# Kernel optimization log

Hardware: AMD Instinct MI355X
Metric: run time of the kernel (lower is better)

The kernel has to match this reference:

```python
import jax, jax.numpy as jnp
import numpy as np

EPS = 1e-5

def layer_norm(x, w, b):
    mu = jnp.mean(x, axis=-1, keepdims=True)
    var = jnp.mean(jnp.square(x - mu), axis=-1, keepdims=True)
    return (x - mu) * jax.lax.rsqrt(var + EPS) * w + b

def setup_inputs() -> dict:
    key = jax.random.key(0)
    ks = jax.random.split(key, 8)
    B, T, C = 8, 512, 768
    s = 1.0 / np.sqrt(C)
    s4 = 1.0 / np.sqrt(4 * C)
    return {
        "x": jax.random.normal(ks[0], (B, T, C), dtype=jnp.float32),
        "ln1_w": jnp.ones((C,), jnp.float32),
        "ln1_b": jnp.zeros((C,), jnp.float32),
        "Wr": jax.random.normal(ks[1], (C, C), dtype=jnp.float32) * s,
        "Wk": jax.random.normal(ks[2], (C, C), dtype=jnp.float32) * s,
        "Wv": jax.random.normal(ks[3], (C, C), dtype=jnp.float32) * s,
        "time_mix_w": jnp.ones((C,), jnp.float32),  # torch init: torch.ones(n_embd)
        "Wrouter": jax.random.normal(ks[4], (C, C), dtype=jnp.float32) * s,
        "ln2_w": jnp.ones((C,), jnp.float32),
        "ln2_b": jnp.zeros((C,), jnp.float32),
        "Wck": jax.random.normal(ks[5], (4 * C, C), dtype=jnp.float32) * s,
        "Wcv": jax.random.normal(ks[6], (C, 4 * C), dtype=jnp.float32) * s4,
    }

def reference(x, ln1_w, ln1_b, Wr, Wk, Wv, time_mix_w, Wrouter, ln2_w, ln2_b, Wck, Wcv):
    B, T, C = x.shape
    xx = layer_norm(x, ln1_w, ln1_b)
    r = xx @ Wr.T
    k = xx @ Wk.T
    v = xx @ Wv.T
    w = -jnp.exp(time_mix_w)                        # (C,) negative per-channel decay rate
    idx = jnp.arange(T)
    diff = jnp.clip(idx[:, None] - idx[None, :], 0).astype(x.dtype)  # (T,T) t-j clamped at 0
    causal = jnp.tril(jnp.ones((T, T), x.dtype))
    decay = jnp.exp(w[:, None, None] * diff[None]) * causal          # (C,T,T)
    kv = k * v                                                       # (B,T,C)
    # wkv[b,t,c] = sum_j decay[c,t,j] * kv[b,j,c]
    wkv = jnp.einsum('ctj,bjc->btc', decay, kv)
    routed_wkv = wkv * jax.nn.sigmoid(xx @ Wrouter.T)
    x = x + r * routed_wkv
    xx2 = layer_norm(x, ln2_w, ln2_b)
    k_cm = jnp.square(jax.nn.relu(xx2 @ Wck.T))                      # (B,T,4C)
    return x + k_cm @ Wcv.T
```

## Files before the change

### kernel.cpp

```cpp
#include <hip/hip_runtime.h>
#include <hip/hip_bf16.h>

typedef __bf16 bf16_t;
typedef __bf16 bf16x8 __attribute__((ext_vector_type(8)));
typedef __bf16 bf16x4 __attribute__((ext_vector_type(4)));
typedef __bf16 bf16x2 __attribute__((ext_vector_type(2)));
typedef float  f32x4  __attribute__((ext_vector_type(4)));

#define LN_EPS 1e-5f


typedef __attribute__((address_space(1))) void gvoid_t;
typedef __attribute__((address_space(3))) void lvoid_t;
__device__ __forceinline__ void glds16(const void* g, void* l) {
    __builtin_amdgcn_global_load_lds((gvoid_t*)g, (lvoid_t*)l, 16, 0, 0);
}

__global__ __launch_bounds__(256) void k_cvt4(const float* __restrict__ s0,
                                              const float* __restrict__ s1,
                                              const float* __restrict__ s2,
                                              const float* __restrict__ s3,
                                              bf16_t* __restrict__ dst, int n4) {
    const float* s = (blockIdx.y == 0) ? s0 : (blockIdx.y == 1) ? s1 : (blockIdx.y == 2) ? s2 : s3;
    bf16_t* d = dst + (size_t)blockIdx.y * ((size_t)n4 * 4);
    int i = blockIdx.x * 256 + threadIdx.x;
    if (i < n4) {
        float4 v = ((const float4*)s)[i];
        bf16x4 o;
        o.x = (bf16_t)v.x; o.y = (bf16_t)v.y; o.z = (bf16_t)v.z; o.w = (bf16_t)v.w;
        ((bf16x4*)d)[i] = o;
    }
}

__global__ __launch_bounds__(256) void k_cvt2(const float* __restrict__ s0,
                                              const float* __restrict__ s1,
                                              bf16_t* __restrict__ dst, int n4) {
    const float* s = (blockIdx.y == 0) ? s0 : s1;
    bf16_t* d = dst + (size_t)blockIdx.y * ((size_t)n4 * 4);
    int i = blockIdx.x * 256 + threadIdx.x;
    if (i < n4) {
        float4 v = ((const float4*)s)[i];
        bf16x4 o;
        o.x = (bf16_t)v.x; o.y = (bf16_t)v.y; o.z = (bf16_t)v.z; o.w = (bf16_t)v.w;
        ((bf16x4*)d)[i] = o;
    }
}

__global__ __launch_bounds__(256) void k_ln(const float* __restrict__ x,
                                            const float* __restrict__ w,
                                            const float* __restrict__ b,
                                            bf16_t* __restrict__ out, int C) {
    int row = blockIdx.x;
    const float* xr = x + (long)row * C;
    int tid = threadIdx.x;
    float s = 0.f, s2 = 0.f;
    for (int i = tid; i < C; i += 256) { float v = xr[i]; s += v; s2 += v * v; }
    for (int m = 32; m; m >>= 1) { s += __shfl_xor(s, m, 64); s2 += __shfl_xor(s2, m, 64); }
    __shared__ float red[8];
    int wv = tid >> 6;
    if ((tid & 63) == 0) { red[wv] = s; red[4 + wv] = s2; }
    __syncthreads();
    float ts  = red[0] + red[1] + red[2] + red[3];
    float ts2 = red[4] + red[5] + red[6] + red[7];
    float mu  = ts / C;
    float var = ts2 / C - mu * mu;
    float rstd = rsqrtf(var + LN_EPS);
    bf16_t* orow = out + (long)row * C;
    for (int i = tid; i < C; i += 256)
        orow[i] = (bf16_t)((xr[i] - mu) * rstd * w[i] + b[i]);
}

template <int EPI>
__global__ __launch_bounds__(256, 6) void k_gemm_bt(const bf16_t* __restrict__ A,
                                                    const bf16_t* __restrict__ Bw,
                                                    void* __restrict__ Cout,
                                                    int N, int Ktot, int nbn, int nks) {
    constexpr int ABUF = 64 * 32;
    constexpr int BBUF = 128 * 32;
    __shared__ __align__(16) bf16_t As[2][64][32];
    __shared__ __align__(16) bf16_t Bs[2][128][32];
    const int tid  = threadIdx.x;
    const int lane = tid & 63, wid = tid >> 6;
    const int wm = (wid >> 1) * 32, wn = (wid & 1) * 64;

    int bid = blockIdx.x;
    int xcd = bid & 7, loc = bid >> 3;
    int bm  = (xcd >> 1) * 16 + loc / 12;
    int cix = (xcd & 1) * 12 + loc % 12;
    int ks  = cix / nbn;
    int bn  = cix % nbn;

    const int fr = lane & 15;
    const int swcol = (((lane >> 4) ^ (lane >> 2)) & 3) * 8;

    f32x4 acc[2][4];
#pragma unroll
    for (int i = 0; i < 2; i++)
#pragma unroll
        for (int j = 0; j < 4; j++) acc[i][j] = (f32x4){0.f, 0.f, 0.f, 0.f};

    const int rsub = lane >> 2;
    const int scol = (((lane & 3) ^ (lane >> 4)) & 3) * 8;
    const bf16_t* Ag = A  + (size_t)(bm * 64  + wid * 16 + rsub) * Ktot + (size_t)ks * 768 + scol;
    const bf16_t* Bg = Bw + (size_t)(bn * 128 + wid * 32 + rsub) * Ktot + (size_t)ks * 768 + scol;
    const size_t Kt16 = (size_t)16 * Ktot;
    bf16_t* lA = &As[0][wid * 16][0];
    bf16_t* lB = &Bs[0][wid * 32][0];

#define STAGE(buf, kt)                                            \
    do {                                                          \
        const bf16_t* a0 = Ag + (size_t)(kt) * 32;                \
        const bf16_t* b0 = Bg + (size_t)(kt) * 32;                \
        glds16(a0,        lA + (buf) * ABUF);                     \
        glds16(b0,        lB + (buf) * BBUF);                     \
        glds16(b0 + Kt16, lB + (buf) * BBUF + 16 * 32);           \
    } while (0)

#define COMPUTE(buf)                                                                         \
    do {                                                                                     \
        const bf16_t* pA = &As[0][0][0] + (buf) * ABUF + (wm + fr) * 32 + swcol;             \
        const bf16_t* pB = &Bs[0][0][0] + (buf) * BBUF + (wn + fr) * 32 + swcol;             \
        bf16x8 af[2], bfr[4];                                                                \
        _Pragma("unroll")                                                                    \
        for (int mi = 0; mi < 2; mi++) af[mi] = *(const bf16x8*)(pA + mi * 512);             \
        _Pragma("unroll")                                                                    \
        for (int ni = 0; ni < 4; ni++) bfr[ni] = *(const bf16x8*)(pB + ni * 512);            \
        __builtin_amdgcn_s_setprio(1);                                                       \
        _Pragma("unroll")                                                                    \
        for (int mi = 0; mi < 2; mi++)                                                       \
            _Pragma("unroll")                                                                \
            for (int ni = 0; ni < 4; ni++)                                                   \
                acc[mi][ni] = __builtin_amdgcn_mfma_f32_16x16x32_bf16(af[mi], bfr[ni], acc[mi][ni], 0, 0, 0); \
        __builtin_amdgcn_s_setprio(0);                                                       \
    } while (0)

    STAGE(0, 0);
    __syncthreads();
    int cur = 0;
    for (int kt = 0; kt < 23; ++kt) {
        STAGE(cur ^ 1, kt + 1);
        COMPUTE(cur);
        __syncthreads();
        cur ^= 1;
    }
    COMPUTE(cur);

#undef STAGE
#undef COMPUTE

    const int row0 = bm * 64 + wm, col0 = bn * 128 + wn;
#pragma unroll
    for (int mi = 0; mi < 2; mi++) {
#pragma unroll
        for (int ni = 0; ni < 4; ni++) {
            int row = row0 + mi * 16 + (lane >> 4) * 4;
            int col = col0 + ni * 16 + (lane & 15);
#pragma unroll
            for (int r = 0; r < 4; r++) {
                float val = acc[mi][ni][r];
                size_t off = (size_t)(row + r) * N + col;
                if (EPI == 0) {
                    ((bf16_t*)Cout)[off] = (bf16_t)val;
                } else if (EPI == 1) {
                    float t = fmaxf(val, 0.f);
                    ((bf16_t*)Cout)[off] = (bf16_t)(t * t);
                } else {
                    atomicAdd(&((float*)Cout)[off], val);
                }
            }
        }
    }
}

__global__ __launch_bounds__(256) void k_scan_local(const bf16_t* __restrict__ y4,
                                                    const float* __restrict__ tmw,
                                                    float* __restrict__ wkvl,
                                                    float* __restrict__ states) {
    int idx = blockIdx.x * 256 + threadIdx.x;
    int cp  = idx % 384;
    int rem = idx / 384;
    int ch  = rem & 15;
    int b   = rem >> 4;
    int c   = cp * 2;
    float d0 = expf(-expf(tmw[c]));
    float d1 = expf(-expf(tmw[c + 1]));
    const bf16_t* base = y4 + ((size_t)(b * 512 + ch * 32)) * 3072 + c;
    float*        wout = wkvl + ((size_t)(b * 512 + ch * 32)) * 768 + c;
    float s0 = 0.f, s1 = 0.f;
#pragma unroll 4
    for (int i = 0; i < 32; i++) {
        bf16x2 k2 = *(const bf16x2*)(base + (size_t)i * 3072 + 768);
        bf16x2 v2 = *(const bf16x2*)(base + (size_t)i * 3072 + 1536);
        s0 = s0 * d0 + (float)k2.x * (float)v2.x;
        s1 = s1 * d1 + (float)k2.y * (float)v2.y;
        *(float2*)(wout + (size_t)i * 768) = make_float2(s0, s1);
    }
    *(float2*)(states + ((size_t)(b * 16 + ch)) * 768 + c) = make_float2(s0, s1);
}

__global__ __launch_bounds__(256) void k_scan_carry(const float* __restrict__ states,
                                                    const float* __restrict__ tmw,
                                                    float* __restrict__ carries) {
    int idx = blockIdx.x * 256 + threadIdx.x;
    int c = idx % 768, b = idx / 768;
    float dL = expf(-expf(tmw[c]) * 32.f);
    float s = 0.f;
    for (int ch = 0; ch < 16; ch++) {
        size_t o = ((size_t)(b * 16 + ch)) * 768 + c;
        carries[o] = s;
        s = s * dL + states[o];
    }
}

__global__ __launch_bounds__(256) void k_mix_ln(const bf16_t* __restrict__ y4,
                                                const float* __restrict__ wkvl,
                                                const float* __restrict__ carries,
                                                const float* __restrict__ tmw,
                                                const float* __restrict__ x,
                                                const float* __restrict__ w2,
                                                const float* __restrict__ b2,
                                                float* __restrict__ out,
                                                bf16_t* __restrict__ xx2) {
    int bt = blockIdx.x;
    int t = bt & 511, b = bt >> 9;
    int tid = threadIdx.x;
    const bf16_t* yrow = y4 + (size_t)bt * 3072;
    const float*  wl   = wkvl + (size_t)bt * 768;
    const float*  cr   = carries + ((size_t)(b * 16) + (t >> 5)) * 768;
    const float*  xr   = x + (size_t)bt * 768;
    float tn = (float)((t & 31) + 1);

    float vals[3];
    float s = 0.f, s2 = 0.f;
#pragma unroll
    for (int j = 0; j < 3; j++) {
        int c = tid + j * 256;
        float rr = (float)yrow[c];
        float gg = (float)yrow[c + 2304];
        float wk = wl[c] + cr[c] * expf(-expf(tmw[c]) * tn);
        float sig = 1.f / (1.f + expf(-gg));
        float o = fmaf(rr, wk * sig, xr[c]);
        vals[j] = o; s += o; s2 += o * o;
    }
    for (int m = 32; m; m >>= 1) { s += __shfl_xor(s, m, 64); s2 += __shfl_xor(s2, m, 64); }
    __shared__ float red[8];
    int wv = tid >> 6;
    if ((tid & 63) == 0) { red[wv] = s; red[4 + wv] = s2; }
    __syncthreads();
    float ts  = red[0] + red[1] + red[2] + red[3];
    float ts2 = red[4] + red[5] + red[6] + red[7];
    float mu  = ts * (1.f / 768.f);
    float var = ts2 * (1.f / 768.f) - mu * mu;
    float rstd = rsqrtf(var + LN_EPS);
    float* orow = out + (size_t)bt * 768;
    bf16_t* xo = xx2 + (size_t)bt * 768;
#pragma unroll
    for (int j = 0; j < 3; j++) {
        int c = tid + j * 256;
        orow[c] = vals[j];
        xo[c] = (bf16_t)((vals[j] - mu) * rstd * w2[c] + b2[c]);
    }
}

extern "C" void kernel_launch(void* const* d_in, const int* in_sizes, int n_in,
                              void* d_out, int out_size, void* d_ws, size_t ws_size,
                              hipStream_t stream) {
    const float* x    = (const float*)d_in[0];
    const float* ln1w = (const float*)d_in[1];
    const float* ln1b = (const float*)d_in[2];
    const float* Wr   = (const float*)d_in[3];
    const float* Wk   = (const float*)d_in[4];
    const float* Wv   = (const float*)d_in[5];
    const float* tmw  = (const float*)d_in[6];
    const float* Wrt  = (const float*)d_in[7];
    const float* ln2w = (const float*)d_in[8];
    const float* ln2b = (const float*)d_in[9];
    const float* Wck  = (const float*)d_in[10];
    const float* Wcv  = (const float*)d_in[11];
    float* out = (float*)d_out;
    char* ws = (char*)d_ws;

    bf16_t* xx     = (bf16_t*)(ws + 0);
    bf16_t* wcat   = (bf16_t*)(ws + 6291456);
    bf16_t* wckb   = (bf16_t*)(ws + 11010048);
    bf16_t* wcvb   = (bf16_t*)(ws + 15728640);
    bf16_t* y4     = (bf16_t*)(ws + 20447232);
    bf16_t* kcm    = (bf16_t*)(ws + 20447232);
    float*  wkvl   = (float*)(ws + 70778880);
    float*  states = (float*)(ws + 83361792);
    float*  carr   = (float*)(ws + 83755008);

    const int n768 = 768 * 768 / 4;
    const int nbig = 3072 * 768 / 4;
    k_cvt4<<<dim3(576, 4), dim3(256), 0, stream>>>(Wr, Wk, Wv, Wrt, wcat, n768);
    k_cvt2<<<dim3(2304, 2), dim3(256), 0, stream>>>(Wck, Wcv, wckb, nbig);

    k_ln<<<dim3(4096), dim3(256), 0, stream>>>(x, ln1w, ln1b, xx, 768);

    k_gemm_bt<0><<<dim3(1536), dim3(256), 0, stream>>>(xx, wcat, (void*)y4, 3072, 768, 24, 1);

    k_scan_local<<<dim3(192), dim3(256), 0, stream>>>(y4, tmw, wkvl, states);
    k_scan_carry<<<dim3(24), dim3(256), 0, stream>>>(states, tmw, carr);
    k_mix_ln<<<dim3(4096), dim3(256), 0, stream>>>(y4, wkvl, carr, tmw, x, ln2w, ln2b, out, xx);

    k_gemm_bt<1><<<dim3(1536), dim3(256), 0, stream>>>(xx, wckb, (void*)kcm, 3072, 768, 24, 1);

    k_gemm_bt<3><<<dim3(1536), dim3(256), 0, stream>>>(kcm, wcvb, (void*)out, 768, 3072, 6, 4);
}
```

Baseline: 179.7 us.

## Enlarge GEMM tiles to 256x256x64 with 512-thread blocks

```diff
diff --git a/kernel.cpp b/kernel.cpp
--- a/kernel.cpp
+++ b/kernel.cpp
@@ -71,63 +71,69 @@
 }
 
 template <int EPI>
-__global__ __launch_bounds__(256, 6) void k_gemm_bt(const bf16_t* __restrict__ A,
+__global__ __launch_bounds__(512, 2) void k_gemm_bt(const bf16_t* __restrict__ A,
                                                     const bf16_t* __restrict__ Bw,
                                                     void* __restrict__ Cout,
                                                     int N, int Ktot, int nbn, int nks) {
-    constexpr int ABUF = 64 * 32;
-    constexpr int BBUF = 128 * 32;
-    __shared__ __align__(16) bf16_t As[2][64][32];
-    __shared__ __align__(16) bf16_t Bs[2][128][32];
+    constexpr int TBUF = 256 * 64;
+    __shared__ __align__(16) bf16_t As[2][256][64];
+    __shared__ __align__(16) bf16_t Bs[2][256][64];
     const int tid  = threadIdx.x;
     const int lane = tid & 63, wid = tid >> 6;
-    const int wm = (wid >> 1) * 32, wn = (wid & 1) * 64;
+    const int wm = (wid >> 2) * 128, wn = (wid & 3) * 64;
 
     int bid = blockIdx.x;
     int xcd = bid & 7, loc = bid >> 3;
-    int bm  = (xcd >> 1) * 16 + loc / 12;
-    int cix = (xcd & 1) * 12 + loc % 12;
+    int bm  = (xcd >> 1) * 4 + loc / 6;
+    int cix = (xcd & 1) * 6 + loc % 6;
     int ks  = cix / nbn;
     int bn  = cix % nbn;
 
-    const int fr = lane & 15;
-    const int swcol = (((lane >> 4) ^ (lane >> 2)) & 3) * 8;
-
-    f32x4 acc[2][4];
-#pragma unroll
-    for (int i = 0; i < 2; i++)
+    const int fr  = lane & 15;
+    const int oct = lane >> 4;
+    const int ph0 = ((oct)     ^ (fr & 7)) * 8;
+    const int ph1 = ((oct + 4) ^ (fr & 7)) * 8;
+
+    f32x4 acc[8][4];
+#pragma unroll
+    for (int i = 0; i < 8; i++)
 #pragma unroll
         for (int j = 0; j < 4; j++) acc[i][j] = (f32x4){0.f, 0.f, 0.f, 0.f};
 
-    const int rsub = lane >> 2;
-    const int scol = (((lane & 3) ^ (lane >> 4)) & 3) * 8;
-    const bf16_t* Ag = A  + (size_t)(bm * 64  + wid * 16 + rsub) * Ktot + (size_t)ks * 768 + scol;
-    const bf16_t* Bg = Bw + (size_t)(bn * 128 + wid * 32 + rsub) * Ktot + (size_t)ks * 768 + scol;
-    const size_t Kt16 = (size_t)16 * Ktot;
-    bf16_t* lA = &As[0][wid * 16][0];
-    bf16_t* lB = &Bs[0][wid * 32][0];
-
-#define STAGE(buf, kt)                                            \
-    do {                                                          \
-        const bf16_t* a0 = Ag + (size_t)(kt) * 32;                \
-        const bf16_t* b0 = Bg + (size_t)(kt) * 32;                \
-        glds16(a0,        lA + (buf) * ABUF);                     \
-        glds16(b0,        lB + (buf) * BBUF);                     \
-        glds16(b0 + Kt16, lB + (buf) * BBUF + 16 * 32);           \
+    const int srow = wid * 32 + (lane >> 3);
+    const int scol = ((lane & 7) ^ (lane >> 3)) * 8;
+    const size_t ksoff = (size_t)ks * 768;
+    const bf16_t* Ag = A  + (size_t)(bm * 256 + srow) * Ktot + ksoff + scol;
+    const bf16_t* Bg = Bw + (size_t)(bn * 256 + srow) * Ktot + ksoff + scol;
+    const size_t Kt8 = (size_t)8 * Ktot;
+    bf16_t* lA = &As[0][0][0] + (size_t)(wid * 32) * 64;
+    bf16_t* lB = &Bs[0][0][0] + (size_t)(wid * 32) * 64;
+
+#define STAGE(buf, kt)                                                     \
+    do {                                                                   \
+        const bf16_t* a0 = Ag + (size_t)(kt) * 64;                         \
+        const bf16_t* b0 = Bg + (size_t)(kt) * 64;                         \
+        _Pragma("unroll")                                                  \
+        for (int q = 0; q < 4; q++) {                                      \
+            glds16(a0 + q * Kt8, lA + (buf) * TBUF + q * 512);             \
+            glds16(b0 + q * Kt8, lB + (buf) * TBUF + q * 512);             \
+        }                                                                  \
     } while (0)
 
-#define COMPUTE(buf)                                                                         \
+#define COMPUTE_KK(buf, PH, KOFF)                                                            \
     do {                                                                                     \
-        const bf16_t* pA = &As[0][0][0] + (buf) * ABUF + (wm + fr) * 32 + swcol;             \
-        const bf16_t* pB = &Bs[0][0][0] + (buf) * BBUF + (wn + fr) * 32 + swcol;             \
-        bf16x8 af[2], bfr[4];                                                                \
+        const bf16_t* bA = &As[0][0][0] + (buf) * TBUF;                                      \
+        const bf16_t* bB = &Bs[0][0][0] + (buf) * TBUF;                                      \
+        bf16x8 bfr[4], af[8];                                                                \
         _Pragma("unroll")                                                                    \
-        for (int mi = 0; mi < 2; mi++) af[mi] = *(const bf16x8*)(pA + mi * 512);             \
+        for (int ni = 0; ni < 4; ni++)                                                       \
+            bfr[ni] = *(const bf16x8*)(bB + (wn + ni * 16 + fr) * 64 + (PH));                \
         _Pragma("unroll")                                                                    \
-        for (int ni = 0; ni < 4; ni++) bfr[ni] = *(const bf16x8*)(pB + ni * 512);            \
+        for (int mi = 0; mi < 8; mi++)                                                       \
+            af[mi] = *(const bf16x8*)(bA + (wm + mi * 16 + fr) * 64 + (PH));                 \
         __builtin_amdgcn_s_setprio(1);                                                       \
         _Pragma("unroll")                                                                    \
-        for (int mi = 0; mi < 2; mi++)                                                       \
+        for (int mi = 0; mi < 8; mi++)                                                       \
             _Pragma("unroll")                                                                \
             for (int ni = 0; ni < 4; ni++)                                                   \
                 acc[mi][ni] = __builtin_amdgcn_mfma_f32_16x16x32_bf16(af[mi], bfr[ni], acc[mi][ni], 0, 0, 0); \
@@ -135,22 +141,22 @@
     } while (0)
 
     STAGE(0, 0);
-    __syncthreads();
-    int cur = 0;
-    for (int kt = 0; kt < 23; ++kt) {
-        STAGE(cur ^ 1, kt + 1);
-        COMPUTE(cur);
-        __syncthreads();
-        cur ^= 1;
-    }
-    COMPUTE(cur);
+    for (int t = 0; t < 12; ++t) {
+        asm volatile("s_waitcnt vmcnt(0)" ::: "memory");
+        __builtin_amdgcn_s_barrier();
+        __builtin_amdgcn_sched_barrier(0);
+        if (t < 11) STAGE((t + 1) & 1, t + 1);
+        __builtin_amdgcn_sched_barrier(0);
+        COMPUTE_KK(t & 1, ph0, 0);
+        COMPUTE_KK(t & 1, ph1, 32);
+    }
 
 #undef STAGE
-#undef COMPUTE
-
-    const int row0 = bm * 64 + wm, col0 = bn * 128 + wn;
-#pragma unroll
-    for (int mi = 0; mi < 2; mi++) {
+#undef COMPUTE_KK
+
+    const int row0 = bm * 256 + wm, col0 = bn * 256 + wn;
+#pragma unroll
+    for (int mi = 0; mi < 8; mi++) {
 #pragma unroll
         for (int ni = 0; ni < 4; ni++) {
             int row = row0 + mi * 16 + (lane >> 4) * 4;
@@ -297,13 +303,13 @@
 
     k_ln<<<dim3(4096), dim3(256), 0, stream>>>(x, ln1w, ln1b, xx, 768);
 
-    k_gemm_bt<0><<<dim3(1536), dim3(256), 0, stream>>>(xx, wcat, (void*)y4, 3072, 768, 24, 1);
+    k_gemm_bt<0><<<dim3(192), dim3(512), 0, stream>>>(xx, wcat, (void*)y4, 3072, 768, 12, 1);
 
     k_scan_local<<<dim3(192), dim3(256), 0, stream>>>(y4, tmw, wkvl, states);
     k_scan_carry<<<dim3(24), dim3(256), 0, stream>>>(states, tmw, carr);
     k_mix_ln<<<dim3(4096), dim3(256), 0, stream>>>(y4, wkvl, carr, tmw, x, ln2w, ln2b, out, xx);
 
-    k_gemm_bt<1><<<dim3(1536), dim3(256), 0, stream>>>(xx, wckb, (void*)kcm, 3072, 768, 24, 1);
-
-    k_gemm_bt<3><<<dim3(1536), dim3(256), 0, stream>>>(kcm, wcvb, (void*)out, 768, 3072, 6, 4);
-}
+    k_gemm_bt<1><<<dim3(192), dim3(512), 0, stream>>>(xx, wckb, (void*)kcm, 3072, 768, 12, 1);
+
+    k_gemm_bt<3><<<dim3(192), dim3(512), 0, stream>>>(kcm, wcvb, (void*)out, 768, 3072, 3, 4);
+}
```

Result: faster. 164.4 us (-8.5%).

## Use 128x128 GEMM tiles with register-staged double-buffered LDS loads

Applied to the files above, without the earlier changes.

```diff
diff --git a/kernel.cpp b/kernel.cpp
--- a/kernel.cpp
+++ b/kernel.cpp
@@ -9,12 +9,6 @@
 
 #define LN_EPS 1e-5f
 
-
-typedef __attribute__((address_space(1))) void gvoid_t;
-typedef __attribute__((address_space(3))) void lvoid_t;
-__device__ __forceinline__ void glds16(const void* g, void* l) {
-    __builtin_amdgcn_global_load_lds((gvoid_t*)g, (lvoid_t*)l, 16, 0, 0);
-}
 
 __global__ __launch_bounds__(256) void k_cvt4(const float* __restrict__ s0,
                                               const float* __restrict__ s1,
@@ -71,86 +65,106 @@
 }
 
 template <int EPI>
-__global__ __launch_bounds__(256, 6) void k_gemm_bt(const bf16_t* __restrict__ A,
+__global__ __launch_bounds__(256, 3) void k_gemm_rs(const bf16_t* __restrict__ A,
                                                     const bf16_t* __restrict__ Bw,
                                                     void* __restrict__ Cout,
                                                     int N, int Ktot, int nbn, int nks) {
-    constexpr int ABUF = 64 * 32;
-    constexpr int BBUF = 128 * 32;
-    __shared__ __align__(16) bf16_t As[2][64][32];
+    __shared__ __align__(16) bf16_t As[2][128][32];
     __shared__ __align__(16) bf16_t Bs[2][128][32];
     const int tid  = threadIdx.x;
     const int lane = tid & 63, wid = tid >> 6;
-    const int wm = (wid >> 1) * 32, wn = (wid & 1) * 64;
+    const int wm = (wid >> 1) * 64, wn = (wid & 1) * 64;
 
     int bid = blockIdx.x;
     int xcd = bid & 7, loc = bid >> 3;
-    int bm  = (xcd >> 1) * 16 + loc / 12;
+    int bm  = (xcd >> 1) * 8 + loc / 12;
     int cix = (xcd & 1) * 12 + loc % 12;
     int ks  = cix / nbn;
     int bn  = cix % nbn;
 
-    const int fr = lane & 15;
-    const int swcol = (((lane >> 4) ^ (lane >> 2)) & 3) * 8;
-
-    f32x4 acc[2][4];
-#pragma unroll
-    for (int i = 0; i < 2; i++)
+    const int fr  = lane & 15;
+    const int swk = (((lane >> 4) ^ (fr & 3) ^ (fr >> 2)) & 3) * 8;
+
+    f32x4 acc[4][4];
+#pragma unroll
+    for (int i = 0; i < 4; i++)
 #pragma unroll
         for (int j = 0; j < 4; j++) acc[i][j] = (f32x4){0.f, 0.f, 0.f, 0.f};
 
-    const int rsub = lane >> 2;
-    const int scol = (((lane & 3) ^ (lane >> 4)) & 3) * 8;
-    const bf16_t* Ag = A  + (size_t)(bm * 64  + wid * 16 + rsub) * Ktot + (size_t)ks * 768 + scol;
-    const bf16_t* Bg = Bw + (size_t)(bn * 128 + wid * 32 + rsub) * Ktot + (size_t)ks * 768 + scol;
-    const size_t Kt16 = (size_t)16 * Ktot;
-    bf16_t* lA = &As[0][wid * 16][0];
-    bf16_t* lB = &Bs[0][wid * 32][0];
-
-#define STAGE(buf, kt)                                            \
-    do {                                                          \
-        const bf16_t* a0 = Ag + (size_t)(kt) * 32;                \
-        const bf16_t* b0 = Bg + (size_t)(kt) * 32;                \
-        glds16(a0,        lA + (buf) * ABUF);                     \
-        glds16(b0,        lB + (buf) * BBUF);                     \
-        glds16(b0 + Kt16, lB + (buf) * BBUF + 16 * 32);           \
+    const int srow = tid & 127;
+    const int sl0  = (tid >> 7) * 2;
+    const int f_r  = (srow & 3) ^ ((srow >> 2) & 3);
+    const int wph0 = ((sl0 ^ f_r) & 3) * 8;
+    const int wph1 = (((sl0 + 1) ^ f_r) & 3) * 8;
+    const size_t ksoff = (size_t)ks * 768;
+    const bf16_t* gA = A  + (size_t)(bm * 128 + srow) * Ktot + ksoff + sl0 * 8;
+    const bf16_t* gB = Bw + (size_t)(bn * 128 + srow) * Ktot + ksoff + sl0 * 8;
+
+    uint4 rA0, rA1, rB0, rB1;
+
+#define LOADREG(kt)                                                  \
+    do {                                                             \
+        const bf16_t* a = gA + (size_t)(kt) * 32;                    \
+        const bf16_t* b = gB + (size_t)(kt) * 32;                    \
+        rA0 = *(const uint4*)(a);                                    \
+        rA1 = *(const uint4*)(a + 8);                                \
+        rB0 = *(const uint4*)(b);                                    \
+        rB1 = *(const uint4*)(b + 8);                                \
+    } while (0)
+
+#define WRITE(buf)                                                   \
+    do {                                                             \
+        *(uint4*)&As[buf][srow][wph0] = rA0;                         \
+        *(uint4*)&As[buf][srow][wph1] = rA1;                         \
+        *(uint4*)&Bs[buf][srow][wph0] = rB0;                         \
+        *(uint4*)&Bs[buf][srow][wph1] = rB1;                         \
     } while (0)
 
 #define COMPUTE(buf)                                                                         \
     do {                                                                                     \
-        const bf16_t* pA = &As[0][0][0] + (buf) * ABUF + (wm + fr) * 32 + swcol;             \
-        const bf16_t* pB = &Bs[0][0][0] + (buf) * BBUF + (wn + fr) * 32 + swcol;             \
-        bf16x8 af[2], bfr[4];                                                                \
+        bf16x8 af[4], bfr[4];                                                                \
         _Pragma("unroll")                                                                    \
-        for (int mi = 0; mi < 2; mi++) af[mi] = *(const bf16x8*)(pA + mi * 512);             \
+        for (int mi = 0; mi < 4; mi++) af[mi] = *(const bf16x8*)&As[buf][wm + mi * 16 + fr][swk]; \
         _Pragma("unroll")                                                                    \
-        for (int ni = 0; ni < 4; ni++) bfr[ni] = *(const bf16x8*)(pB + ni * 512);            \
+        for (int ni = 0; ni < 4; ni++) bfr[ni] = *(const bf16x8*)&Bs[buf][wn + ni * 16 + fr][swk]; \
         __builtin_amdgcn_s_setprio(1);                                                       \
         _Pragma("unroll")                                                                    \
-        for (int mi = 0; mi < 2; mi++)                                                       \
+        for (int mi = 0; mi < 4; mi++)                                                       \
             _Pragma("unroll")                                                                \
             for (int ni = 0; ni < 4; ni++)                                                   \
                 acc[mi][ni] = __builtin_amdgcn_mfma_f32_16x16x32_bf16(af[mi], bfr[ni], acc[mi][ni], 0, 0, 0); \
         __builtin_amdgcn_s_setprio(0);                                                       \
     } while (0)
 
-    STAGE(0, 0);
-    __syncthreads();
+#define BAR()                                                        \
+    do {                                                             \
+        asm volatile("s_waitcnt lgkmcnt(0)" ::: "memory");           \
+        __builtin_amdgcn_s_barrier();                                \
+        __builtin_amdgcn_sched_barrier(0);                           \
+    } while (0)
+
+    LOADREG(0);
+    WRITE(0);
+    LOADREG(1);
+    BAR();
+
     int cur = 0;
-    for (int kt = 0; kt < 23; ++kt) {
-        STAGE(cur ^ 1, kt + 1);
+    for (int t = 0; t < 24; ++t) {
+        if (t < 23) WRITE(cur ^ 1);
+        if (t < 22) LOADREG(t + 2);
         COMPUTE(cur);
-        __syncthreads();
+        BAR();
         cur ^= 1;
     }
-    COMPUTE(cur);
-
-#undef STAGE
+
+#undef LOADREG
+#undef WRITE
 #undef COMPUTE
-
-    const int row0 = bm * 64 + wm, col0 = bn * 128 + wn;
-#pragma unroll
-    for (int mi = 0; mi < 2; mi++) {
+#undef BAR
+
+    const int row0 = bm * 128 + wm, col0 = bn * 128 + wn;
+#pragma unroll
+    for (int mi = 0; mi < 4; mi++) {
 #pragma unroll
         for (int ni = 0; ni < 4; ni++) {
             int row = row0 + mi * 16 + (lane >> 4) * 4;
@@ -297,13 +311,13 @@
 
     k_ln<<<dim3(4096), dim3(256), 0, stream>>>(x, ln1w, ln1b, xx, 768);
 
-    k_gemm_bt<0><<<dim3(1536), dim3(256), 0, stream>>>(xx, wcat, (void*)y4, 3072, 768, 24, 1);
+    k_gemm_rs<0><<<dim3(768), dim3(256), 0, stream>>>(xx, wcat, (void*)y4, 3072, 768, 24, 1);
 
     k_scan_local<<<dim3(192), dim3(256), 0, stream>>>(y4, tmw, wkvl, states);
     k_scan_carry<<<dim3(24), dim3(256), 0, stream>>>(states, tmw, carr);
     k_mix_ln<<<dim3(4096), dim3(256), 0, stream>>>(y4, wkvl, carr, tmw, x, ln2w, ln2b, out, xx);
 
-    k_gemm_bt<1><<<dim3(1536), dim3(256), 0, stream>>>(xx, wckb, (void*)kcm, 3072, 768, 24, 1);
-
-    k_gemm_bt<3><<<dim3(1536), dim3(256), 0, stream>>>(kcm, wcvb, (void*)out, 768, 3072, 6, 4);
-}
+    k_gemm_rs<1><<<dim3(768), dim3(256), 0, stream>>>(xx, wckb, (void*)kcm, 3072, 768, 24, 1);
+
+    k_gemm_rs<3><<<dim3(768), dim3(256), 0, stream>>>(kcm, wcvb, (void*)out, 768, 3072, 6, 4);
+}
```

After: 198.6 us. 10.6% more time.

## Rewrite GEMMs with B slab resident in LDS and A streamed from registers

Applied to the files above, without the earlier changes.

```diff
diff --git a/kernel.cpp b/kernel.cpp
--- a/kernel.cpp
+++ b/kernel.cpp
@@ -9,12 +9,6 @@
 
 #define LN_EPS 1e-5f
 
-
-typedef __attribute__((address_space(1))) void gvoid_t;
-typedef __attribute__((address_space(3))) void lvoid_t;
-__device__ __forceinline__ void glds16(const void* g, void* l) {
-    __builtin_amdgcn_global_load_lds((gvoid_t*)g, (lvoid_t*)l, 16, 0, 0);
-}
 
 __global__ __launch_bounds__(256) void k_cvt4(const float* __restrict__ s0,
                                               const float* __restrict__ s1,
@@ -71,90 +65,94 @@
 }
 
 template <int EPI>
-__global__ __launch_bounds__(256, 6) void k_gemm_bt(const bf16_t* __restrict__ A,
-                                                    const bf16_t* __restrict__ Bw,
-                                                    void* __restrict__ Cout,
-                                                    int N, int Ktot, int nbn, int nks) {
-    constexpr int ABUF = 64 * 32;
-    constexpr int BBUF = 128 * 32;
-    __shared__ __align__(16) bf16_t As[2][64][32];
-    __shared__ __align__(16) bf16_t Bs[2][128][32];
+__global__ __launch_bounds__(512, 2) void k_gemm_bstat(const bf16_t* __restrict__ A,
+                                                       const bf16_t* __restrict__ Bw,
+                                                       void* __restrict__ Cout,
+                                                       int N, int Ktot, int nks) {
+    __shared__ __align__(16) bf16_t Bs[96][768];
     const int tid  = threadIdx.x;
     const int lane = tid & 63, wid = tid >> 6;
-    const int wm = (wid >> 1) * 32, wn = (wid & 1) * 64;
+    const int gm = wid >> 1, gn = wid & 1;
+    const int fr = lane & 15, ko = lane >> 4;
 
     int bid = blockIdx.x;
     int xcd = bid & 7, loc = bid >> 3;
-    int bm  = (xcd >> 1) * 16 + loc / 12;
-    int cix = (xcd & 1) * 12 + loc % 12;
-    int ks  = cix / nbn;
-    int bn  = cix % nbn;
-
-    const int fr = lane & 15;
-    const int swcol = (((lane >> 4) ^ (lane >> 2)) & 3) * 8;
-
-    f32x4 acc[2][4];
-#pragma unroll
-    for (int i = 0; i < 2; i++)
-#pragma unroll
-        for (int j = 0; j < 4; j++) acc[i][j] = (f32x4){0.f, 0.f, 0.f, 0.f};
-
-    const int rsub = lane >> 2;
-    const int scol = (((lane & 3) ^ (lane >> 4)) & 3) * 8;
-    const bf16_t* Ag = A  + (size_t)(bm * 64  + wid * 16 + rsub) * Ktot + (size_t)ks * 768 + scol;
-    const bf16_t* Bg = Bw + (size_t)(bn * 128 + wid * 32 + rsub) * Ktot + (size_t)ks * 768 + scol;
-    const size_t Kt16 = (size_t)16 * Ktot;
-    bf16_t* lA = &As[0][wid * 16][0];
-    bf16_t* lB = &Bs[0][wid * 32][0];
-
-#define STAGE(buf, kt)                                            \
-    do {                                                          \
-        const bf16_t* a0 = Ag + (size_t)(kt) * 32;                \
-        const bf16_t* b0 = Bg + (size_t)(kt) * 32;                \
-        glds16(a0,        lA + (buf) * ABUF);                     \
-        glds16(b0,        lB + (buf) * BBUF);                     \
-        glds16(b0 + Kt16, lB + (buf) * BBUF + 16 * 32);           \
+    int mc  = (xcd & 3) * 2 + (loc >> 4);
+    int ci  = (xcd >> 2) * 16 + (loc & 15);
+    int bn  = ci / nks, ks = ci % nks;
+
+    {
+        const bf16_t* gb = Bw + (size_t)(bn * 96) * Ktot + (size_t)ks * 768;
+#pragma unroll
+        for (int i = 0; i < 18; ++i) {
+            int idx = tid + i * 512;
+            int r = idx / 96, s = idx % 96;
+            uint4 v = *(const uint4*)(gb + (size_t)r * Ktot + s * 8);
+            *(uint4*)&Bs[r][(s ^ (r & 7)) * 8] = v;
+        }
+    }
+
+    f32x4 acc[8][3];
+#pragma unroll
+    for (int i = 0; i < 8; i++)
+#pragma unroll
+        for (int j = 0; j < 3; j++) acc[i][j] = (f32x4){0.f, 0.f, 0.f, 0.f};
+
+    const int rbase = mc * 512 + gm * 128;
+    const bf16_t* ga = A + (size_t)(rbase + fr) * Ktot + (size_t)ks * 768 + ko * 8;
+    const size_t rs16 = (size_t)16 * Ktot;
+    const int rb = gn * 48;
+    const int f8 = fr & 7;
+
+    __syncthreads();
+
+#define LOADA(dst, kt)                                                          \
+    do {                                                                        \
+        _Pragma("unroll")                                                       \
+        for (int mi = 0; mi < 8; ++mi)                                          \
+            dst[mi] = *(const bf16x8*)(ga + (size_t)mi * rs16 + (kt) * 32);     \
     } while (0)
 
-#define COMPUTE(buf)                                                                         \
+#define READB(bf, kt)                                                           \
+    do {                                                                        \
+        _Pragma("unroll")                                                       \
+        for (int ni = 0; ni < 3; ++ni)                                          \
+            bf[ni] = *(const bf16x8*)&Bs[rb + ni * 16 + fr][(((kt) * 4 + ko) ^ f8) * 8]; \
+    } while (0)
+
+#define MFMAB(af, bf)                                                                        \
     do {                                                                                     \
-        const bf16_t* pA = &As[0][0][0] + (buf) * ABUF + (wm + fr) * 32 + swcol;             \
-        const bf16_t* pB = &Bs[0][0][0] + (buf) * BBUF + (wn + fr) * 32 + swcol;             \
-        bf16x8 af[2], bfr[4];                                                                \
-        _Pragma("unroll")                                                                    \
-        for (int mi = 0; mi < 2; mi++) af[mi] = *(const bf16x8*)(pA + mi * 512);             \
-        _Pragma("unroll")                                                                    \
-        for (int ni = 0; ni < 4; ni++) bfr[ni] = *(const bf16x8*)(pB + ni * 512);            \
         __builtin_amdgcn_s_setprio(1);                                                       \
         _Pragma("unroll")                                                                    \
-        for (int mi = 0; mi < 2; mi++)                                                       \
+        for (int mi = 0; mi < 8; ++mi)                                                       \
             _Pragma("unroll")                                                                \
-            for (int ni = 0; ni < 4; ni++)                                                   \
-                acc[mi][ni] = __builtin_amdgcn_mfma_f32_16x16x32_bf16(af[mi], bfr[ni], acc[mi][ni], 0, 0, 0); \
+            for (int ni = 0; ni < 3; ++ni)                                                   \
+                acc[mi][ni] = __builtin_amdgcn_mfma_f32_16x16x32_bf16(af[mi], bf[ni], acc[mi][ni], 0, 0, 0); \
         __builtin_amdgcn_s_setprio(0);                                                       \
     } while (0)
 
-    STAGE(0, 0);
-    __syncthreads();
-    int cur = 0;
-    for (int kt = 0; kt < 23; ++kt) {
-        STAGE(cur ^ 1, kt + 1);
-        COMPUTE(cur);
-        __syncthreads();
-        cur ^= 1;
-    }
-    COMPUTE(cur);
-
-#undef STAGE
-#undef COMPUTE
-
-    const int row0 = bm * 64 + wm, col0 = bn * 128 + wn;
-#pragma unroll
-    for (int mi = 0; mi < 2; mi++) {
-#pragma unroll
-        for (int ni = 0; ni < 4; ni++) {
-            int row = row0 + mi * 16 + (lane >> 4) * 4;
-            int col = col0 + ni * 16 + (lane & 15);
+    bf16x8 afA[8], afB[8], bfr[3];
+    LOADA(afA, 0);
+    for (int kt = 0; kt < 24; kt += 2) {
+        LOADA(afB, kt + 1);
+        READB(bfr, kt);
+        MFMAB(afA, bfr);
+        if (kt + 2 < 24) LOADA(afA, kt + 2);
+        READB(bfr, kt + 1);
+        MFMAB(afB, bfr);
+    }
+
+#undef LOADA
+#undef READB
+#undef MFMAB
+
+    const int col0 = bn * 96 + rb;
+#pragma unroll
+    for (int mi = 0; mi < 8; mi++) {
+#pragma unroll
+        for (int ni = 0; ni < 3; ni++) {
+            int row = rbase + mi * 16 + ko * 4;
+            int col = col0 + ni * 16 + fr;
 #pragma unroll
             for (int r = 0; r < 4; r++) {
                 float val = acc[mi][ni][r];
@@ -297,13 +295,13 @@
 
     k_ln<<<dim3(4096), dim3(256), 0, stream>>>(x, ln1w, ln1b, xx, 768);
 
-    k_gemm_bt<0><<<dim3(1536), dim3(256), 0, stream>>>(xx, wcat, (void*)y4, 3072, 768, 24, 1);
+    k_gemm_bstat<0><<<dim3(256), dim3(512), 0, stream>>>(xx, wcat, (void*)y4, 3072, 768, 1);
 
     k_scan_local<<<dim3(192), dim3(256), 0, stream>>>(y4, tmw, wkvl, states);
     k_scan_carry<<<dim3(24), dim3(256), 0, stream>>>(states, tmw, carr);
     k_mix_ln<<<dim3(4096), dim3(256), 0, stream>>>(y4, wkvl, carr, tmw, x, ln2w, ln2b, out, xx);
 
-    k_gemm_bt<1><<<dim3(1536), dim3(256), 0, stream>>>(xx, wckb, (void*)kcm, 3072, 768, 24, 1);
-
-    k_gemm_bt<3><<<dim3(1536), dim3(256), 0, stream>>>(kcm, wcvb, (void*)out, 768, 3072, 6, 4);
-}
+    k_gemm_bstat<1><<<dim3(256), dim3(512), 0, stream>>>(xx, wckb, (void*)kcm, 3072, 768, 1);
+
+    k_gemm_bstat<3><<<dim3(256), dim3(512), 0, stream>>>(kcm, wcvb, (void*)out, 768, 3072, 4);
+}
```

After: 227.8 us. 1.27x slower.
